# Optimization experiments

Measured on AMD Instinct MI355X. Metric: run time of the kernel, lower is better.

Reference implementation:

```python
import jax, jax.numpy as jnp
import numpy as np

EMBED_DIM = 2048
NUM_HEADS = 16
HEAD_DIM = EMBED_DIM // NUM_HEADS
SCALE = EMBED_DIM ** -0.5  # NOTE: original uses full embed_dim, not head_dim


def setup_inputs() -> dict:
    key = jax.random.key(0)
    ks = jax.random.split(key, 9)
    d = EMBED_DIM
    s = 1.0 / np.sqrt(d)
    inp = {
        "x": jax.random.normal(ks[0], (2, 2048, d), dtype=jnp.float32),
        "wq": jax.random.uniform(ks[1], (d, d), jnp.float32, -s, s),
        "bq": jnp.zeros((d,), jnp.float32),
        "wk": jax.random.uniform(ks[2], (d, d), jnp.float32, -s, s),
        "bk": jnp.zeros((d,), jnp.float32),
        "wv": jax.random.uniform(ks[3], (d, d), jnp.float32, -s, s),
        "bv": jnp.zeros((d,), jnp.float32),
        "wo": jax.random.uniform(ks[4], (d, d), jnp.float32, -s, s),
        "bo": jnp.zeros((d,), jnp.float32),
    }
    return inp


def reference(x, wq, bq, wk, bk, wv, bv, wo, bo):
    b, t, d = x.shape
    h, hd = NUM_HEADS, HEAD_DIM
    # projections (torch Linear: x @ W.T + b; here weights stored as [in, out])
    q = (x @ wq + bq).reshape(b, t, h, hd).transpose(0, 2, 1, 3)  # [b,h,t,hd]
    k = (x @ wk + bk).reshape(b, t, h, hd).transpose(0, 2, 1, 3)
    v = (x @ wv + bv).reshape(b, t, h, hd).transpose(0, 2, 1, 3)
    scores = jnp.einsum("bhqd,bhkd->bhqk", q, k) * SCALE
    probs = jax.nn.softmax(scores, axis=-1)
    attn = jnp.einsum("bhqk,bhkd->bhqd", probs, v)
    attn = attn.transpose(0, 2, 1, 3).reshape(b, t, d)
    return attn @ wo + bo
```

## Files before the change

kernel.cpp:

```cpp
#include <hip/hip_runtime.h>

typedef unsigned int u32;
typedef __bf16 bf16;
typedef bf16 bf16x4 __attribute__((ext_vector_type(4)));
typedef bf16 bf16x8 __attribute__((ext_vector_type(8)));
typedef float f32x4 __attribute__((ext_vector_type(4)));

#define T_ 2048
#define D_ 2048
#define H_ 16
#define HD_ 128
#define SCALE_ 0.022097086912079608f
#define LOG2E_ 1.4426950408889634f

typedef __attribute__((address_space(1))) u32 gu32;
typedef __attribute__((address_space(3))) u32 lu32;

__device__ __forceinline__ void gload_lds16(const void* g, void* l) {
  __builtin_amdgcn_global_load_lds((gu32*)(void*)g, (lu32*)l, 16, 0, 0);
}

__global__ void cast_x_kernel(const float* __restrict__ x, bf16* __restrict__ xb) {
  int i = blockIdx.x * 256 + threadIdx.x;
  float4 v = ((const float4*)x)[i];
  bf16x4 o;
  o.x = (bf16)v.x; o.y = (bf16)v.y; o.z = (bf16)v.z; o.w = (bf16)v.w;
  ((bf16x4*)xb)[i] = o;
}

__global__ void twcast_kernel(const float* __restrict__ w0, const float* __restrict__ w1,
                              const float* __restrict__ w2, const float* __restrict__ w3,
                              bf16* __restrict__ o0, bf16* __restrict__ o1,
                              bf16* __restrict__ o2, bf16* __restrict__ o3) {
  int z = blockIdx.z;
  const float* W = (z == 0) ? w0 : (z == 1) ? w1 : (z == 2) ? w2 : w3;
  bf16* O = (z == 0) ? o0 : (z == 1) ? o1 : (z == 2) ? o2 : o3;
  __shared__ float tile[64][65];
  int t = threadIdx.x, tx = t & 15, ty = t >> 4;
  int n0 = blockIdx.x * 64, k0 = blockIdx.y * 64;
#pragma unroll
  for (int i = 0; i < 4; i++) {
    float4 v = *(const float4*)&W[(size_t)(k0 + ty + i * 16) * D_ + n0 + tx * 4];
    tile[ty + i * 16][tx * 4 + 0] = v.x;
    tile[ty + i * 16][tx * 4 + 1] = v.y;
    tile[ty + i * 16][tx * 4 + 2] = v.z;
    tile[ty + i * 16][tx * 4 + 3] = v.w;
  }
  __syncthreads();
#pragma unroll
  for (int i = 0; i < 4; i++) {
    int n = ty + i * 16;
    bf16x4 o;
    o.x = (bf16)tile[tx * 4 + 0][n];
    o.y = (bf16)tile[tx * 4 + 1][n];
    o.z = (bf16)tile[tx * 4 + 2][n];
    o.w = (bf16)tile[tx * 4 + 3][n];
    *(bf16x4*)&O[(size_t)(n0 + n) * D_ + k0 + tx * 4] = o;
  }
}

__device__ __forceinline__ void stage_tile(const bf16* __restrict__ A,
                                           const bf16* __restrict__ Bt,
                                           char* aT, char* bT,
                                           int m0, int n0, int k0, int t) {
#pragma unroll
  for (int i = 0; i < 4; i++) {
    int L = i * 4096 + t * 16;
    int row = L >> 7;
    int kb = (L & 127) ^ ((row & 7) << 4);
    gload_lds16(A + (size_t)(m0 + row) * 2048 + k0 + (kb >> 1), aT + L);
    gload_lds16(Bt + (size_t)(n0 + row) * 2048 + k0 + (kb >> 1), bT + L);
  }
}

__device__ __forceinline__ void gemm_compute64(const char* aT, const char* bT,
                                               f32x4 acc[4][4], int lane, int wr, int wc) {
#pragma unroll
  for (int kk = 0; kk < 2; kk++) {
    int ak = kk * 64 + ((lane >> 4) << 4);
    bf16x8 af[4], bfv[4];
#pragma unroll
    for (int f = 0; f < 4; f++) {
      int ar = wr * 64 + f * 16 + (lane & 15);
      af[f] = *(const bf16x8*)(aT + ar * 128 + (ak ^ ((ar & 7) << 4)));
      int br = wc * 64 + f * 16 + (lane & 15);
      bfv[f] = *(const bf16x8*)(bT + br * 128 + (ak ^ ((br & 7) << 4)));
    }
#pragma unroll
    for (int mi = 0; mi < 4; mi++)
#pragma unroll
      for (int ni = 0; ni < 4; ni++)
        acc[mi][ni] = __builtin_amdgcn_mfma_f32_16x16x32_bf16(af[mi], bfv[ni], acc[mi][ni], 0, 0, 0);
  }
}

__device__ __forceinline__ void gemm_core_128(const bf16* __restrict__ A,
                                              const bf16* __restrict__ Bt,
                                              f32x4 acc[4][4], int m0, int n0) {
  __shared__ char smem[65536];
  const int t = threadIdx.x;
  const int lane = t & 63;
  const int wr = (t >> 7) & 1;
  const int wc = (t >> 6) & 1;
  stage_tile(A, Bt, smem, smem + 16384, m0, n0, 0, t);
  __syncthreads();
  int cur = 0;
  for (int k0 = 64; k0 < 2048; k0 += 64) {
    char* base = smem + (cur ^ 1) * 32768;
    stage_tile(A, Bt, base, base + 16384, m0, n0, k0, t);
    char* cbase = smem + cur * 32768;
    gemm_compute64(cbase, cbase + 16384, acc, lane, wr, wc);
    __syncthreads();
    cur ^= 1;
  }
  char* cbase = smem + cur * 32768;
  gemm_compute64(cbase, cbase + 16384, acc, lane, wr, wc);
}

__global__ __launch_bounds__(256, 2) void qkv_gemm_kernel(
    const bf16* __restrict__ xb,
    const bf16* __restrict__ wqt, const bf16* __restrict__ wkt, const bf16* __restrict__ wvt,
    const float* __restrict__ bq, const float* __restrict__ bk, const float* __restrict__ bv,
    bf16* __restrict__ Qb, bf16* __restrict__ Kb, bf16* __restrict__ Vb) {
  const bf16* Bt; const float* bias; bf16* Out; float scale;
  int z = blockIdx.z;
  if (z == 0)      { Bt = wqt; bias = bq; Out = Qb; scale = SCALE_ * LOG2E_; }
  else if (z == 1) { Bt = wkt; bias = bk; Out = Kb; scale = 1.0f; }
  else             { Bt = wvt; bias = bv; Out = Vb; scale = 1.0f; }
  int m0 = blockIdx.y * 128, n0 = blockIdx.x * 128;
  f32x4 zero = {0.f, 0.f, 0.f, 0.f};
  f32x4 acc[4][4];
#pragma unroll
  for (int mi = 0; mi < 4; mi++)
#pragma unroll
    for (int ni = 0; ni < 4; ni++) acc[mi][ni] = zero;
  gemm_core_128(xb, Bt, acc, m0, n0);
  int lane = threadIdx.x & 63;
  int wr = (threadIdx.x >> 7) & 1, wc = (threadIdx.x >> 6) & 1;
#pragma unroll
  for (int ni = 0; ni < 4; ni++) {
    int cn = n0 + wc * 64 + ni * 16 + (lane & 15);
    float bb = bias[cn];
    int h = cn >> 7, hd = cn & 127;
#pragma unroll
    for (int mi = 0; mi < 4; mi++) {
      int rm = m0 + wr * 64 + mi * 16 + ((lane >> 4) << 2);
#pragma unroll
      for (int r = 0; r < 4; r++) {
        int mg = rm + r;
        int b = mg >> 11, tt = mg & 2047;
        Out[(size_t)((b * H_ + h) * T_ + tt) * HD_ + hd] = (bf16)((acc[mi][ni][r] + bb) * scale);
      }
    }
  }
}

__global__ void vtr_kernel(const bf16* __restrict__ V, bf16* __restrict__ Vt) {
  __shared__ bf16 tile[64][72];
  int t = threadIdx.x, tx = t & 15, ty = t >> 4;
  int t0 = blockIdx.x * 64, hd0 = blockIdx.y * 64, bh = blockIdx.z;
  const bf16* Vi = V + (size_t)bh * T_ * HD_;
  bf16* Vo = Vt + (size_t)bh * HD_ * T_;
#pragma unroll
  for (int i = 0; i < 4; i++) {
    bf16x4 v = *(const bf16x4*)&Vi[(size_t)(t0 + ty + i * 16) * HD_ + hd0 + tx * 4];
    tile[ty + i * 16][tx * 4 + 0] = v.x;
    tile[ty + i * 16][tx * 4 + 1] = v.y;
    tile[ty + i * 16][tx * 4 + 2] = v.z;
    tile[ty + i * 16][tx * 4 + 3] = v.w;
  }
  __syncthreads();
#pragma unroll
  for (int i = 0; i < 4; i++) {
    int hd = ty + i * 16;
    bf16x4 v;
    v.x = tile[tx * 4 + 0][hd];
    v.y = tile[tx * 4 + 1][hd];
    v.z = tile[tx * 4 + 2][hd];
    v.w = tile[tx * 4 + 3][hd];
    *(bf16x4*)&Vo[(size_t)(hd0 + hd) * T_ + t0 + tx * 4] = v;
  }
}

__global__ __launch_bounds__(256, 4) void attn_kernel(
    const bf16* __restrict__ Qb, const bf16* __restrict__ Kb,
    const bf16* __restrict__ Vtb, bf16* __restrict__ Ab) {
  __shared__ char smem[40960];
  char* Klds = smem;
  char* Vlds = smem + 16384;
  char* Plds = smem + 32768;
  const int t = threadIdx.x, lane = t & 63, w = t >> 6;
  const int bh = blockIdx.y;
  const int q0 = blockIdx.x * 64;
  const bf16* Qh = Qb + (size_t)bh * T_ * HD_;
  const bf16* Kh = Kb + (size_t)bh * T_ * HD_;
  const bf16* Vh = Vtb + (size_t)bh * HD_ * T_;

  bf16x8 qf[4];
#pragma unroll
  for (int kf = 0; kf < 4; kf++) {
    int row = q0 + w * 16 + (lane & 15);
    int hd = kf * 32 + ((lane >> 4) << 3);
    qf[kf] = *(const bf16x8*)(Qh + (size_t)row * HD_ + hd);
  }

  f32x4 zero = {0.f, 0.f, 0.f, 0.f};
  f32x4 o[8];
#pragma unroll
  for (int nf = 0; nf < 8; nf++) o[nf] = zero;
  float mrow[4], lrow[4];
#pragma unroll
  for (int r = 0; r < 4; r++) { mrow[r] = -1e30f; lrow[r] = 0.f; }

  for (int kt = 0; kt < T_; kt += 64) {
#pragma unroll
    for (int i = 0; i < 4; i++) {
      int L = i * 4096 + t * 16;
      int rowK = L >> 8;
      int kbK = (L & 255) ^ ((rowK & 7) << 4);
      gload_lds16(Kh + (size_t)(kt + rowK) * HD_ + (kbK >> 1), Klds + L);
      int rowV = L >> 7;
      int kbV = (L & 127) ^ ((rowV & 7) << 4);
      gload_lds16(Vh + (size_t)rowV * T_ + kt + (kbV >> 1), Vlds + L);
    }
    __syncthreads();

    f32x4 s[4];
#pragma unroll
    for (int nf = 0; nf < 4; nf++) s[nf] = zero;
#pragma unroll
    for (int kf = 0; kf < 4; kf++) {
      int kb = kf * 64 + ((lane >> 4) << 4);
      bf16x8 kfr[4];
#pragma unroll
      for (int nf = 0; nf < 4; nf++) {
        int rr = nf * 16 + (lane & 15);
        kfr[nf] = *(const bf16x8*)(Klds + rr * 256 + (kb ^ ((rr & 7) << 4)));
      }
#pragma unroll
      for (int nf = 0; nf < 4; nf++)
        s[nf] = __builtin_amdgcn_mfma_f32_16x16x32_bf16(qf[kf], kfr[nf], s[nf], 0, 0, 0);
    }

#pragma unroll
    for (int r = 0; r < 4; r++) {
      float mx = fmaxf(fmaxf(s[0][r], s[1][r]), fmaxf(s[2][r], s[3][r]));
      mx = fmaxf(mx, __shfl_xor(mx, 1));
      mx = fmaxf(mx, __shfl_xor(mx, 2));
      mx = fmaxf(mx, __shfl_xor(mx, 4));
      mx = fmaxf(mx, __shfl_xor(mx, 8));
      if (mx > mrow[r] + 8.f) {
        float fac = exp2f(mrow[r] - mx);
        mrow[r] = mx;
        lrow[r] *= fac;
#pragma unroll
        for (int nf = 0; nf < 8; nf++) o[nf][r] *= fac;
      }
      float m = mrow[r];
      float rs = 0.f;
#pragma unroll
      for (int nf = 0; nf < 4; nf++) {
        float p = exp2f(s[nf][r] - m);
        s[nf][r] = p;
        rs += p;
      }
      rs += __shfl_xor(rs, 1);
      rs += __shfl_xor(rs, 2);
      rs += __shfl_xor(rs, 4);
      rs += __shfl_xor(rs, 8);
      lrow[r] += rs;
      int row = w * 16 + ((lane >> 4) << 2) + r;
#pragma unroll
      for (int nf = 0; nf < 4; nf++) {
        int cb = (nf * 32 + (lane & 15) * 2) ^ ((row & 7) << 4);
        *(bf16*)(Plds + row * 128 + cb) = (bf16)s[nf][r];
      }
    }

#pragma unroll
    for (int kf = 0; kf < 2; kf++) {
      int kb = kf * 64 + ((lane >> 4) << 4);
      int rr = w * 16 + (lane & 15);
      bf16x8 pf = *(const bf16x8*)(Plds + rr * 128 + (kb ^ ((rr & 7) << 4)));
#pragma unroll
      for (int nf = 0; nf < 8; nf++) {
        int vr = nf * 16 + (lane & 15);
        bf16x8 vf = *(const bf16x8*)(Vlds + vr * 128 + (kb ^ ((vr & 7) << 4)));
        o[nf] = __builtin_amdgcn_mfma_f32_16x16x32_bf16(pf, vf, o[nf], 0, 0, 0);
      }
    }
    __syncthreads();
  }

  int b = bh >> 4, h = bh & 15;
#pragma unroll
  for (int r = 0; r < 4; r++) {
    float inv = 1.f / lrow[r];
    int tq = q0 + w * 16 + ((lane >> 4) << 2) + r;
    size_t base = ((size_t)b * T_ + tq) * D_ + h * HD_;
#pragma unroll
    for (int nf = 0; nf < 8; nf++) {
      int hd = nf * 16 + (lane & 15);
      Ab[base + hd] = (bf16)(o[nf][r] * inv);
    }
  }
}

__global__ __launch_bounds__(256, 2) void out_gemm_kernel(
    const bf16* __restrict__ Ab, const bf16* __restrict__ wot,
    const float* __restrict__ bo, float* __restrict__ out) {
  int m0 = blockIdx.y * 128, n0 = blockIdx.x * 128;
  f32x4 zero = {0.f, 0.f, 0.f, 0.f};
  f32x4 acc[4][4];
#pragma unroll
  for (int mi = 0; mi < 4; mi++)
#pragma unroll
    for (int ni = 0; ni < 4; ni++) acc[mi][ni] = zero;
  gemm_core_128(Ab, wot, acc, m0, n0);
  int lane = threadIdx.x & 63;
  int wr = (threadIdx.x >> 7) & 1, wc = (threadIdx.x >> 6) & 1;
#pragma unroll
  for (int ni = 0; ni < 4; ni++) {
    int cn = n0 + wc * 64 + ni * 16 + (lane & 15);
    float bb = bo[cn];
#pragma unroll
    for (int mi = 0; mi < 4; mi++) {
      int rm = m0 + wr * 64 + mi * 16 + ((lane >> 4) << 2);
#pragma unroll
      for (int r = 0; r < 4; r++)
        out[(size_t)(rm + r) * D_ + cn] = acc[mi][ni][r] + bb;
    }
  }
}

extern "C" void kernel_launch(void* const* d_in, const int* in_sizes, int n_in,
                              void* d_out, int out_size, void* d_ws, size_t ws_size,
                              hipStream_t stream) {
  const float* x  = (const float*)d_in[0];
  const float* wq = (const float*)d_in[1];
  const float* bq = (const float*)d_in[2];
  const float* wk = (const float*)d_in[3];
  const float* bk = (const float*)d_in[4];
  const float* wv = (const float*)d_in[5];
  const float* bv = (const float*)d_in[6];
  const float* wo = (const float*)d_in[7];
  const float* bo = (const float*)d_in[8];
  float* out = (float*)d_out;
  char* ws = (char*)d_ws;

  bf16* xb  = (bf16*)(ws);
  bf16* wqt = (bf16*)(ws + 16777216);
  bf16* wkt = (bf16*)(ws + 25165824);
  bf16* wvt = (bf16*)(ws + 33554432);
  bf16* wot = (bf16*)(ws + 41943040);
  bf16* Qb  = (bf16*)(ws + 50331648);
  bf16* Kb  = (bf16*)(ws + 67108864);
  bf16* Vb  = (bf16*)(ws + 83886080);
  bf16* Vtb = (bf16*)(ws + 100663296);
  bf16* Ab  = xb;

  cast_x_kernel<<<8192, 256, 0, stream>>>(x, xb);
  twcast_kernel<<<dim3(32, 32, 4), 256, 0, stream>>>(wq, wk, wv, wo, wqt, wkt, wvt, wot);
  qkv_gemm_kernel<<<dim3(16, 32, 3), 256, 0, stream>>>(xb, wqt, wkt, wvt, bq, bk, bv, Qb, Kb, Vb);
  vtr_kernel<<<dim3(32, 2, 32), 256, 0, stream>>>(Vb, Vtb);
  attn_kernel<<<dim3(32, 32), 256, 0, stream>>>(Qb, Kb, Vtb, Ab);
  out_gemm_kernel<<<dim3(16, 32), 256, 0, stream>>>(Ab, wot, bo, out);

  (void)in_sizes; (void)n_in; (void)out_size; (void)ws_size;
}
```

Measured before the change: 462.6 us.

## Rewrite attention with 32x32 MFMA, register-resident P, fuse V transpose into QKV GEMM

The attention kernel now has each wave handle 32 query rows using 32x32x16 MFMA in transposed form (S^T = K·Q^T). This lets each lane own one query row, so softmax max/sum need only one cross-half shuffle. The P tile is repacked into MFMA operands with shuffles instead of a round trip through LDS. The QKV GEMM epilogue writes V already transposed, which removes the separate transpose kernel and its buffer. In exchange, occupancy drops (launch bounds 2, 128 queries per block, fewer blocks), and the transposed V store is strided and poorly coalesced.

```diff
diff --git a/kernel.cpp b/kernel.cpp
--- a/kernel.cpp
+++ b/kernel.cpp
@@ -2,9 +2,12 @@
 
 typedef unsigned int u32;
 typedef __bf16 bf16;
+typedef bf16 bf16x2 __attribute__((ext_vector_type(2)));
 typedef bf16 bf16x4 __attribute__((ext_vector_type(4)));
 typedef bf16 bf16x8 __attribute__((ext_vector_type(8)));
 typedef float f32x4 __attribute__((ext_vector_type(4)));
+typedef float f32x16 __attribute__((ext_vector_type(16)));
+typedef u32 u32x4 __attribute__((ext_vector_type(4)));
 
 #define T_ 2048
 #define D_ 2048
@@ -18,6 +21,12 @@
 
 __device__ __forceinline__ void gload_lds16(const void* g, void* l) {
   __builtin_amdgcn_global_load_lds((gu32*)(void*)g, (lu32*)l, 16, 0, 0);
+}
+
+__device__ __forceinline__ u32 packbf(float a, float b) {
+  union { bf16x2 v; u32 u; } c;
+  c.v.x = (bf16)a; c.v.y = (bf16)b;
+  return c.u;
 }
 
 __global__ void cast_x_kernel(const float* __restrict__ x, bf16* __restrict__ xb) {
@@ -121,12 +130,12 @@
     const bf16* __restrict__ xb,
     const bf16* __restrict__ wqt, const bf16* __restrict__ wkt, const bf16* __restrict__ wvt,
     const float* __restrict__ bq, const float* __restrict__ bk, const float* __restrict__ bv,
-    bf16* __restrict__ Qb, bf16* __restrict__ Kb, bf16* __restrict__ Vb) {
-  const bf16* Bt; const float* bias; bf16* Out; float scale;
+    bf16* __restrict__ Qb, bf16* __restrict__ Kb, bf16* __restrict__ Vtb) {
+  const bf16* Bt; const float* bias; float scale;
   int z = blockIdx.z;
-  if (z == 0)      { Bt = wqt; bias = bq; Out = Qb; scale = SCALE_ * LOG2E_; }
-  else if (z == 1) { Bt = wkt; bias = bk; Out = Kb; scale = 1.0f; }
-  else             { Bt = wvt; bias = bv; Out = Vb; scale = 1.0f; }
+  if (z == 0)      { Bt = wqt; bias = bq; scale = SCALE_ * LOG2E_; }
+  else if (z == 1) { Bt = wkt; bias = bk; scale = 1.0f; }
+  else             { Bt = wvt; bias = bv; scale = 1.0f; }
   int m0 = blockIdx.y * 128, n0 = blockIdx.x * 128;
   f32x4 zero = {0.f, 0.f, 0.f, 0.f};
   f32x4 acc[4][4];
@@ -137,80 +146,73 @@
   gemm_core_128(xb, Bt, acc, m0, n0);
   int lane = threadIdx.x & 63;
   int wr = (threadIdx.x >> 7) & 1, wc = (threadIdx.x >> 6) & 1;
-#pragma unroll
-  for (int ni = 0; ni < 4; ni++) {
-    int cn = n0 + wc * 64 + ni * 16 + (lane & 15);
-    float bb = bias[cn];
-    int h = cn >> 7, hd = cn & 127;
-#pragma unroll
-    for (int mi = 0; mi < 4; mi++) {
-      int rm = m0 + wr * 64 + mi * 16 + ((lane >> 4) << 2);
-#pragma unroll
-      for (int r = 0; r < 4; r++) {
-        int mg = rm + r;
-        int b = mg >> 11, tt = mg & 2047;
-        Out[(size_t)((b * H_ + h) * T_ + tt) * HD_ + hd] = (bf16)((acc[mi][ni][r] + bb) * scale);
-      }
-    }
-  }
-}
-
-__global__ void vtr_kernel(const bf16* __restrict__ V, bf16* __restrict__ Vt) {
-  __shared__ bf16 tile[64][72];
-  int t = threadIdx.x, tx = t & 15, ty = t >> 4;
-  int t0 = blockIdx.x * 64, hd0 = blockIdx.y * 64, bh = blockIdx.z;
-  const bf16* Vi = V + (size_t)bh * T_ * HD_;
-  bf16* Vo = Vt + (size_t)bh * HD_ * T_;
-#pragma unroll
-  for (int i = 0; i < 4; i++) {
-    bf16x4 v = *(const bf16x4*)&Vi[(size_t)(t0 + ty + i * 16) * HD_ + hd0 + tx * 4];
-    tile[ty + i * 16][tx * 4 + 0] = v.x;
-    tile[ty + i * 16][tx * 4 + 1] = v.y;
-    tile[ty + i * 16][tx * 4 + 2] = v.z;
-    tile[ty + i * 16][tx * 4 + 3] = v.w;
-  }
-  __syncthreads();
-#pragma unroll
-  for (int i = 0; i < 4; i++) {
-    int hd = ty + i * 16;
-    bf16x4 v;
-    v.x = tile[tx * 4 + 0][hd];
-    v.y = tile[tx * 4 + 1][hd];
-    v.z = tile[tx * 4 + 2][hd];
-    v.w = tile[tx * 4 + 3][hd];
-    *(bf16x4*)&Vo[(size_t)(hd0 + hd) * T_ + t0 + tx * 4] = v;
-  }
-}
-
-__global__ __launch_bounds__(256, 4) void attn_kernel(
+  if (z < 2) {
+    bf16* Out = (z == 0) ? Qb : Kb;
+#pragma unroll
+    for (int ni = 0; ni < 4; ni++) {
+      int cn = n0 + wc * 64 + ni * 16 + (lane & 15);
+      float bb = bias[cn];
+      int h = cn >> 7, hd = cn & 127;
+#pragma unroll
+      for (int mi = 0; mi < 4; mi++) {
+        int rm = m0 + wr * 64 + mi * 16 + ((lane >> 4) << 2);
+#pragma unroll
+        for (int r = 0; r < 4; r++) {
+          int mg = rm + r;
+          int b = mg >> 11, tt = mg & 2047;
+          Out[(size_t)((b * H_ + h) * T_ + tt) * HD_ + hd] = (bf16)((acc[mi][ni][r] + bb) * scale);
+        }
+      }
+    }
+  } else {
+#pragma unroll
+    for (int ni = 0; ni < 4; ni++) {
+      int cn = n0 + wc * 64 + ni * 16 + (lane & 15);
+      float bb = bias[cn];
+      int h = cn >> 7, hd = cn & 127;
+#pragma unroll
+      for (int mi = 0; mi < 4; mi++) {
+        int rm = m0 + wr * 64 + mi * 16 + ((lane >> 4) << 2);
+        int b = rm >> 11, tt = rm & 2047;
+        bf16x4 st;
+        st.x = (bf16)(acc[mi][ni][0] + bb);
+        st.y = (bf16)(acc[mi][ni][1] + bb);
+        st.z = (bf16)(acc[mi][ni][2] + bb);
+        st.w = (bf16)(acc[mi][ni][3] + bb);
+        *(bf16x4*)&Vtb[((size_t)(b * H_ + h) * HD_ + hd) * T_ + tt] = st;
+      }
+    }
+  }
+}
+
+__global__ __launch_bounds__(256, 2) void attn_kernel(
     const bf16* __restrict__ Qb, const bf16* __restrict__ Kb,
     const bf16* __restrict__ Vtb, bf16* __restrict__ Ab) {
-  __shared__ char smem[40960];
+  __shared__ char smem[32768];
   char* Klds = smem;
   char* Vlds = smem + 16384;
-  char* Plds = smem + 32768;
   const int t = threadIdx.x, lane = t & 63, w = t >> 6;
+  const int h0 = lane >> 5;
+  const int q = lane & 31;
   const int bh = blockIdx.y;
-  const int q0 = blockIdx.x * 64;
+  const int q0 = blockIdx.x * 128;
   const bf16* Qh = Qb + (size_t)bh * T_ * HD_;
   const bf16* Kh = Kb + (size_t)bh * T_ * HD_;
   const bf16* Vh = Vtb + (size_t)bh * HD_ * T_;
 
-  bf16x8 qf[4];
-#pragma unroll
-  for (int kf = 0; kf < 4; kf++) {
-    int row = q0 + w * 16 + (lane & 15);
-    int hd = kf * 32 + ((lane >> 4) << 3);
-    qf[kf] = *(const bf16x8*)(Qh + (size_t)row * HD_ + hd);
-  }
-
-  f32x4 zero = {0.f, 0.f, 0.f, 0.f};
-  f32x4 o[8];
-#pragma unroll
-  for (int nf = 0; nf < 8; nf++) o[nf] = zero;
-  float mrow[4], lrow[4];
-#pragma unroll
-  for (int r = 0; r < 4; r++) { mrow[r] = -1e30f; lrow[r] = 0.f; }
+  bf16x8 qf[8];
+  {
+    const bf16* qrow = Qh + (size_t)(q0 + w * 32 + q) * HD_ + h0 * 8;
+#pragma unroll
+    for (int kf = 0; kf < 8; kf++) qf[kf] = *(const bf16x8*)(qrow + kf * 16);
+  }
+
+  f32x16 o[4];
+#pragma unroll
+  for (int nb = 0; nb < 4; nb++)
+#pragma unroll
+    for (int r = 0; r < 16; r++) o[nb][r] = 0.f;
+  float m = -1e30f, l = 0.f;
 
   for (int kt = 0; kt < T_; kt += 64) {
 #pragma unroll
@@ -225,85 +227,99 @@
     }
     __syncthreads();
 
-    f32x4 s[4];
-#pragma unroll
-    for (int nf = 0; nf < 4; nf++) s[nf] = zero;
-#pragma unroll
-    for (int kf = 0; kf < 4; kf++) {
-      int kb = kf * 64 + ((lane >> 4) << 4);
-      bf16x8 kfr[4];
-#pragma unroll
-      for (int nf = 0; nf < 4; nf++) {
-        int rr = nf * 16 + (lane & 15);
-        kfr[nf] = *(const bf16x8*)(Klds + rr * 256 + (kb ^ ((rr & 7) << 4)));
-      }
-#pragma unroll
-      for (int nf = 0; nf < 4; nf++)
-        s[nf] = __builtin_amdgcn_mfma_f32_16x16x32_bf16(qf[kf], kfr[nf], s[nf], 0, 0, 0);
-    }
-
-#pragma unroll
-    for (int r = 0; r < 4; r++) {
-      float mx = fmaxf(fmaxf(s[0][r], s[1][r]), fmaxf(s[2][r], s[3][r]));
-      mx = fmaxf(mx, __shfl_xor(mx, 1));
-      mx = fmaxf(mx, __shfl_xor(mx, 2));
-      mx = fmaxf(mx, __shfl_xor(mx, 4));
-      mx = fmaxf(mx, __shfl_xor(mx, 8));
-      if (mx > mrow[r] + 8.f) {
-        float fac = exp2f(mrow[r] - mx);
-        mrow[r] = mx;
-        lrow[r] *= fac;
-#pragma unroll
-        for (int nf = 0; nf < 8; nf++) o[nf][r] *= fac;
-      }
-      float m = mrow[r];
-      float rs = 0.f;
-#pragma unroll
-      for (int nf = 0; nf < 4; nf++) {
-        float p = exp2f(s[nf][r] - m);
-        s[nf][r] = p;
+    f32x16 s[2];
+#pragma unroll
+    for (int sub = 0; sub < 2; sub++)
+#pragma unroll
+      for (int r = 0; r < 16; r++) s[sub][r] = 0.f;
+#pragma unroll
+    for (int kf = 0; kf < 8; kf++) {
+#pragma unroll
+      for (int sub = 0; sub < 2; sub++) {
+        int rr = sub * 32 + q;
+        bf16x8 kfr = *(const bf16x8*)(Klds + rr * 256 + ((kf * 32 + h0 * 16) ^ ((rr & 7) << 4)));
+        s[sub] = __builtin_amdgcn_mfma_f32_32x32x16_bf16(kfr, qf[kf], s[sub], 0, 0, 0);
+      }
+    }
+
+    float mx = s[0][0];
+#pragma unroll
+    for (int sub = 0; sub < 2; sub++)
+#pragma unroll
+      for (int r = 0; r < 16; r++) mx = fmaxf(mx, s[sub][r]);
+    mx = fmaxf(mx, __shfl_xor(mx, 32));
+    if (__any(mx > m + 8.f)) {
+      float mn = fmaxf(m, mx);
+      float fac = exp2f(m - mn);
+      m = mn;
+      l *= fac;
+#pragma unroll
+      for (int nb = 0; nb < 4; nb++)
+#pragma unroll
+        for (int r = 0; r < 16; r++) o[nb][r] *= fac;
+    }
+    float rs = 0.f;
+#pragma unroll
+    for (int sub = 0; sub < 2; sub++)
+#pragma unroll
+      for (int r = 0; r < 16; r++) {
+        float p = exp2f(s[sub][r] - m);
+        s[sub][r] = p;
         rs += p;
       }
-      rs += __shfl_xor(rs, 1);
-      rs += __shfl_xor(rs, 2);
-      rs += __shfl_xor(rs, 4);
-      rs += __shfl_xor(rs, 8);
-      lrow[r] += rs;
-      int row = w * 16 + ((lane >> 4) << 2) + r;
-#pragma unroll
-      for (int nf = 0; nf < 4; nf++) {
-        int cb = (nf * 32 + (lane & 15) * 2) ^ ((row & 7) << 4);
-        *(bf16*)(Plds + row * 128 + cb) = (bf16)s[nf][r];
-      }
-    }
-
-#pragma unroll
-    for (int kf = 0; kf < 2; kf++) {
-      int kb = kf * 64 + ((lane >> 4) << 4);
-      int rr = w * 16 + (lane & 15);
-      bf16x8 pf = *(const bf16x8*)(Plds + rr * 128 + (kb ^ ((rr & 7) << 4)));
-#pragma unroll
-      for (int nf = 0; nf < 8; nf++) {
-        int vr = nf * 16 + (lane & 15);
-        bf16x8 vf = *(const bf16x8*)(Vlds + vr * 128 + (kb ^ ((vr & 7) << 4)));
-        o[nf] = __builtin_amdgcn_mfma_f32_16x16x32_bf16(pf, vf, o[nf], 0, 0, 0);
+    rs += __shfl_xor(rs, 32);
+    l += rs;
+
+    bf16x8 pfrag[4];
+#pragma unroll
+    for (int sub = 0; sub < 2; sub++) {
+#pragma unroll
+      for (int c = 0; c < 2; c++) {
+        u32 X0 = packbf(s[sub][8 * c + 0], s[sub][8 * c + 1]);
+        u32 X1 = packbf(s[sub][8 * c + 2], s[sub][8 * c + 3]);
+        u32 Y0 = packbf(s[sub][8 * c + 4], s[sub][8 * c + 5]);
+        u32 Y1 = packbf(s[sub][8 * c + 6], s[sub][8 * c + 7]);
+        u32 sX0 = (u32)__shfl_xor((int)X0, 32);
+        u32 sX1 = (u32)__shfl_xor((int)X1, 32);
+        u32 sY0 = (u32)__shfl_xor((int)Y0, 32);
+        u32 sY1 = (u32)__shfl_xor((int)Y1, 32);
+        u32x4 wv;
+        wv.x = h0 ? sY0 : X0;
+        wv.y = h0 ? sY1 : X1;
+        wv.z = h0 ? Y0 : sX0;
+        wv.w = h0 ? Y1 : sX1;
+        union { u32x4 u; bf16x8 b; } cv;
+        cv.u = wv;
+        pfrag[sub * 2 + c] = cv.b;
+      }
+    }
+
+#pragma unroll
+    for (int nb = 0; nb < 4; nb++) {
+      int vr = nb * 32 + q;
+#pragma unroll
+      for (int ks = 0; ks < 4; ks++) {
+        bf16x8 vf = *(const bf16x8*)(Vlds + vr * 128 + ((ks * 32 + h0 * 16) ^ ((vr & 7) << 4)));
+        o[nb] = __builtin_amdgcn_mfma_f32_32x32x16_bf16(vf, pfrag[ks], o[nb], 0, 0, 0);
       }
     }
     __syncthreads();
   }
 
-  int b = bh >> 4, h = bh & 15;
-#pragma unroll
-  for (int r = 0; r < 4; r++) {
-    float inv = 1.f / lrow[r];
-    int tq = q0 + w * 16 + ((lane >> 4) << 2) + r;
-    size_t base = ((size_t)b * T_ + tq) * D_ + h * HD_;
-#pragma unroll
-    for (int nf = 0; nf < 8; nf++) {
-      int hd = nf * 16 + (lane & 15);
-      Ab[base + hd] = (bf16)(o[nf][r] * inv);
-    }
-  }
+  float inv = 1.f / l;
+  int b = bh >> 4, hh = bh & 15;
+  bf16* orow = Ab + ((size_t)b * T_ + q0 + w * 32 + q) * D_ + hh * HD_;
+#pragma unroll
+  for (int nb = 0; nb < 4; nb++)
+#pragma unroll
+    for (int g = 0; g < 4; g++) {
+      bf16x4 st;
+      st.x = (bf16)(o[nb][4 * g + 0] * inv);
+      st.y = (bf16)(o[nb][4 * g + 1] * inv);
+      st.z = (bf16)(o[nb][4 * g + 2] * inv);
+      st.w = (bf16)(o[nb][4 * g + 3] * inv);
+      *(bf16x4*)(orow + nb * 32 + 8 * g + 4 * h0) = st;
+    }
 }
 
 __global__ __launch_bounds__(256, 2) void out_gemm_kernel(
@@ -355,15 +371,13 @@
   bf16* wot = (bf16*)(ws + 41943040);
   bf16* Qb  = (bf16*)(ws + 50331648);
   bf16* Kb  = (bf16*)(ws + 67108864);
-  bf16* Vb  = (bf16*)(ws + 83886080);
-  bf16* Vtb = (bf16*)(ws + 100663296);
+  bf16* Vtb = (bf16*)(ws + 83886080);
   bf16* Ab  = xb;
 
   cast_x_kernel<<<8192, 256, 0, stream>>>(x, xb);
   twcast_kernel<<<dim3(32, 32, 4), 256, 0, stream>>>(wq, wk, wv, wo, wqt, wkt, wvt, wot);
-  qkv_gemm_kernel<<<dim3(16, 32, 3), 256, 0, stream>>>(xb, wqt, wkt, wvt, bq, bk, bv, Qb, Kb, Vb);
-  vtr_kernel<<<dim3(32, 2, 32), 256, 0, stream>>>(Vb, Vtb);
-  attn_kernel<<<dim3(32, 32), 256, 0, stream>>>(Qb, Kb, Vtb, Ab);
+  qkv_gemm_kernel<<<dim3(16, 32, 3), 256, 0, stream>>>(xb, wqt, wkt, wvt, bq, bk, bv, Qb, Kb, Vtb);
+  attn_kernel<<<dim3(16, 32), 256, 0, stream>>>(Qb, Kb, Vtb, Ab);
   out_gemm_kernel<<<dim3(16, 32), 256, 0, stream>>>(Ab, wot, bo, out);
 
   (void)in_sizes; (void)n_in; (void)out_size; (void)ws_size;
```

After: 387.4 us. 16.3% less time.
